# Kernel tuning notes

Measured on AMD Instinct MI355X. Metric: run time of the kernel, lower is better.

The kernel has to match this reference:

```python
import jax, jax.numpy as jnp
import numpy as np

B, Cin, H, W = 8, 256, 32, 32
KS, NH, K = 32, 8, 5          # key_size == value_size, num_heads, kernel_size
STRIDE, PAD = 1, 2
Cout = KS * 3 * NH            # 768
EPS = 1e-5


def setup_inputs() -> dict:
    key = jax.random.key(0)
    k0, k1, k2 = jax.random.split(key, 3)
    return {
        "x": jax.random.normal(k0, (B, Cin, H, W), jnp.float32),
        "conv_w": jax.random.normal(k1, (Cout, Cin), jnp.float32) / np.sqrt(Cin).astype(np.float32),
        "conv_b": jax.random.normal(k2, (Cout,), jnp.float32) * 0.02,
        "gn_w": jnp.ones((Cout,), jnp.float32),
        "gn_b": jnp.zeros((Cout,), jnp.float32),
    }


def reference(x, conv_w, conv_b, gn_w, gn_b):
    Bb = x.shape[0]
    OH = (H + 2 * PAD - K) // STRIDE + 1
    OW = (W + 2 * PAD - K) // STRIDE + 1

    # 1x1 conv: (B, Cout, H, W)
    attn = jnp.einsum('bchw,oc->bohw', x, conv_w) + conv_b[None, :, None, None]

    # unfold / Tile2d -> (B, KH, KW, Cout, OH, OW)
    ap = jnp.pad(attn, ((0, 0), (0, 0), (PAD, PAD), (PAD, PAD)))
    rows = []
    for kh in range(K):
        cols = [ap[:, :, kh:kh + OH * STRIDE:STRIDE, kw:kw + OW * STRIDE:STRIDE]
                for kw in range(K)]
        rows.append(jnp.stack(cols, axis=1))          # (B, KW, C, OH, OW)
    tiles = jnp.stack(rows, axis=1)                   # (B, KH, KW, C, OH, OW)

    # GroupNorm over (group_channels, OH, OW) per (b, kh, kw) sample.
    # groups = 3*NH, group size = KS (each head's key/query/value chunk).
    G = 3 * NH
    t = tiles.reshape(Bb, K, K, G, KS, OH, OW)
    mean = t.mean(axis=(4, 5, 6), keepdims=True)
    var = t.var(axis=(4, 5, 6), keepdims=True)        # biased, like torch GroupNorm
    t = (t - mean) * jax.lax.rsqrt(var + EPS)
    t = t.reshape(Bb, K, K, Cout, OH, OW)
    t = t * gn_w[None, None, None, :, None, None] + gn_b[None, None, None, :, None, None]

    # (B, OH, OW, NH, 3*KS, KH*KW)
    t = t.transpose(0, 4, 5, 3, 1, 2).reshape(Bb, OH, OW, NH, 3 * KS, K * K)
    keyt = t[..., :KS, :]            # (B, OH, OW, NH, KS, KK)
    qt = t[..., KS:2 * KS, :]
    vt = t[..., 2 * KS:, :]          # (B, OH, OW, NH, VS, KK)

    q = qt.mean(axis=-1)             # mean query over the window: (B, OH, OW, NH, KS)
    sal = jnp.einsum('bijnk,bijnkp->bijnp', q, keyt) / np.float32(np.sqrt(KS))
    mask = jax.nn.softmax(sal, axis=-1)               # (B, OH, OW, NH, KK)
    out = jnp.einsum('bijnvp,bijnp->bijnv', vt, mask)  # (B, OH, OW, NH, VS)

    out = out.transpose(0, 3, 4, 1, 2).reshape(Bb, NH * KS, OH, OW)
    return out
```

## Files before the change

kernel.cpp:

```cpp
#include <hip/hip_runtime.h>
#include <hip/hip_bf16.h>

#define B_    8
#define CIN   256
#define COUT  768
#define G_    24
#define PW    40
#define PLANE 1440
#define EPS_  1e-5f

typedef float f32x4 __attribute__((ext_vector_type(4)));
typedef short s16x8 __attribute__((ext_vector_type(8)));
typedef unsigned short ushort_t;
typedef unsigned short u16x4 __attribute__((ext_vector_type(4)));
typedef unsigned long long ull_t;

static __device__ __forceinline__ ushort_t f2bf(float f) {
    union { float f; unsigned u; } a; a.f = f;
    const unsigned u = a.u;
    const unsigned r = u + 0x7FFFu + ((u >> 16) & 1u);
    return (ushort_t)(r >> 16);
}
static __device__ __forceinline__ float bf2f(ushort_t h) {
    union { unsigned u; float f; } a; a.u = ((unsigned)h) << 16; return a.f;
}

__launch_bounds__(256)
__global__ void prep(const float* __restrict__ x, const float* __restrict__ w,
                     ushort_t* __restrict__ Xt, ushort_t* __restrict__ Wt) {
    const int z = blockIdx.x;
    const int t = threadIdx.x;
    if (z < 2048) {
        __shared__ ushort_t tile[32][33];
        const int b  = z >> 8, rem = z & 255;
        const int k0 = (rem >> 5) * 32, n0 = (rem & 31) * 32;
        const int kk = t >> 5, nn = t & 31;
        #pragma unroll
        for (int it = 0; it < 4; ++it) {
            const int kr = kk + it * 8;
            tile[kr][nn] = f2bf(x[((size_t)(b * 256 + k0 + kr)) * 1024 + n0 + nn]);
        }
        __syncthreads();
        const int kk2 = t & 31, nb = t >> 5;
        #pragma unroll
        for (int it = 0; it < 4; ++it) {
            const int nr = nb + it * 8;
            Xt[((size_t)(b * 1024 + n0 + nr)) * 256 + k0 + kk2] = tile[kk2][nr];
        }
    } else {
        const int idx = (z - 2048) * 256 + t;
        Wt[idx] = f2bf(w[idx]);
    }
}

__launch_bounds__(256)
__global__ void conv_gemm(const ushort_t* __restrict__ Wt, const ushort_t* __restrict__ Xt,
                          const float* __restrict__ bias, ushort_t* __restrict__ attn,
                          float* __restrict__ rowAgg) {
    const int t = threadIdx.x;
    const int wv = t >> 6, lane = t & 63;
    const int q = lane >> 4, l15 = lane & 15;
    const int m0 = blockIdx.y * 64;
    const int mw = wv * 16;
    const int n_t = blockIdx.x * 64;
    const int b = n_t >> 10, nl0 = n_t & 1023;
    const int y0 = nl0 >> 5;

    __shared__ ushort_t Ct[64][2][44];
    __shared__ float red[128][11];

    const ushort_t* aP = Wt + (size_t)(m0 + mw + l15) * 256 + q * 8;
    const ushort_t* bP = Xt + (size_t)(b * 1024 + nl0 + l15) * 256 + q * 8;

    f32x4 acc[4] = {{0,0,0,0},{0,0,0,0},{0,0,0,0},{0,0,0,0}};
    #pragma unroll
    for (int k0 = 0; k0 < 256; k0 += 32) {
        const s16x8 a  = *(const s16x8*)(aP + k0);
        const s16x8 b0 = *(const s16x8*)(bP + k0);
        const s16x8 b1 = *(const s16x8*)(bP + 16 * 256 + k0);
        const s16x8 b2 = *(const s16x8*)(bP + 32 * 256 + k0);
        const s16x8 b3 = *(const s16x8*)(bP + 48 * 256 + k0);
        acc[0] = __builtin_amdgcn_mfma_f32_16x16x32_bf16(a, b0, acc[0], 0, 0, 0);
        acc[1] = __builtin_amdgcn_mfma_f32_16x16x32_bf16(a, b1, acc[1], 0, 0, 0);
        acc[2] = __builtin_amdgcn_mfma_f32_16x16x32_bf16(a, b2, acc[2], 0, 0, 0);
        acc[3] = __builtin_amdgcn_mfma_f32_16x16x32_bf16(a, b3, acc[3], 0, 0, 0);
    }

    float bb[4];
    #pragma unroll
    for (int r = 0; r < 4; ++r) bb[r] = bias[m0 + mw + q * 4 + r];
    #pragma unroll
    for (int j = 0; j < 4; ++j) {
        const int yy = j >> 1, xx = (j & 1) * 16 + l15;
        #pragma unroll
        for (int r = 0; r < 4; ++r)
            Ct[mw + q * 4 + r][yy][2 + xx] = f2bf(acc[j][r] + bb[r]);
    }
    #pragma unroll
    for (int it = 0; it < 2; ++it) {
        const int id = it * 256 + t;
        const int m = id >> 3, yy = (id >> 2) & 1, pos = id & 3;
        const int us = (pos == 0) ? 0 : (32 + 2 * pos);
        *(unsigned*)&Ct[m][yy][us] = 0u;
    }
    __syncthreads();

    ushort_t* pb = attn + ((size_t)(b * COUT + m0)) * PLANE;
    #pragma unroll
    for (int it = 0; it < 5; ++it) {
        const int id = it * 256 + t;
        const int m = id / 20, rem = id % 20, yy = rem / 10, s = rem % 10;
        const ull_t v = *(const ull_t*)&Ct[m][yy][s * 4];
        *(ull_t*)(pb + (size_t)m * PLANE + (y0 + yy + 2) * PW + s * 4) = v;
    }
    if (y0 == 0 || y0 == 30) {
        const int rowA = (y0 == 0) ? 0 : 34;
        #pragma unroll
        for (int it = 0; it < 5; ++it) {
            const int id = it * 256 + t;
            const int m = id / 20, rem = id % 20, yy = rem / 10, s = rem % 10;
            *(ull_t*)(pb + (size_t)m * PLANE + (rowA + yy) * PW + s * 4) = 0ull;
        }
    }

    if (t < 128) {
        const int gi = t >> 6, yy = (t >> 5) & 1, c = t & 31;
        const int m = gi * 32 + c;
        float lin = 0.f, sq = 0.f, e0 = 0.f, e1 = 0.f, e30 = 0.f, e31 = 0.f;
        #pragma unroll
        for (int u = 0; u < 9; ++u) {
            const ull_t vv = *(const ull_t*)&Ct[m][yy][u * 4];
            const unsigned lo = (unsigned)vv, hi = (unsigned)(vv >> 32);
            union { unsigned u; float f; } f0, f1, f2, f3;
            f0.u = lo << 16; f1.u = lo & 0xffff0000u;
            f2.u = hi << 16; f3.u = hi & 0xffff0000u;
            lin += (f0.f + f1.f) + (f2.f + f3.f);
            sq  += (f0.f * f0.f + f1.f * f1.f) + (f2.f * f2.f + f3.f * f3.f);
            if (u == 0) { e0 = f2.f; e1 = f3.f; }
            if (u == 8) { e30 = f0.f; e31 = f1.f; }
        }
        red[t][0] = lin; red[t][1] = sq;
        red[t][2] = e0;  red[t][3] = e0 * e0;
        red[t][4] = e1;  red[t][5] = e1 * e1;
        red[t][6] = e30; red[t][7] = e30 * e30;
        red[t][8] = e31; red[t][9] = e31 * e31;
    }
    __syncthreads();
    if (t < 40) {
        const int s = t % 10, gy = t / 10;
        const int gi = gy >> 1, yy = gy & 1;
        float sum = 0.f;
        #pragma unroll
        for (int c = 0; c < 32; ++c) sum += red[gi * 64 + yy * 32 + c][s];
        const int g = blockIdx.y * 2 + gi;
        rowAgg[(((size_t)b * G_ + g) * 32 + (y0 + yy)) * 10 + s] = sum;
    }
}

__launch_bounds__(64)
__global__ void gnfin(const float* __restrict__ rowAgg,
                      float* __restrict__ meanArr, float* __restrict__ rstdArr) {
    const int bg = blockIdx.x;
    const int t = threadIdx.x;
    __shared__ float rp[32][5], rp2[32][5];
    if (t < 32) {
        const float* a = rowAgg + ((size_t)bg * 32 + t) * 10;
        const float S = a[0], Sq = a[1];
        const float e0 = a[2], q0 = a[3], e1 = a[4], q1 = a[5];
        const float e30 = a[6], q30 = a[7], e31 = a[8], q31 = a[9];
        rp[t][0] = S - e30 - e31; rp[t][1] = S - e31; rp[t][2] = S;
        rp[t][3] = S - e0;        rp[t][4] = S - e0 - e1;
        rp2[t][0] = Sq - q30 - q31; rp2[t][1] = Sq - q31; rp2[t][2] = Sq;
        rp2[t][3] = Sq - q0;        rp2[t][4] = Sq - q0 - q1;
    }
    __syncthreads();
    if (t < 25) {
        const int kw = t % 5, kh = t / 5;
        float cs = 0.f, cs2 = 0.f;
        #pragma unroll
        for (int yy = 0; yy < 32; ++yy) { cs += rp[yy][kw]; cs2 += rp2[yy][kw]; }
        if (kh == 0)      { cs -= rp[30][kw] + rp[31][kw]; cs2 -= rp2[30][kw] + rp2[31][kw]; }
        else if (kh == 1) { cs -= rp[31][kw];              cs2 -= rp2[31][kw]; }
        else if (kh == 3) { cs -= rp[0][kw];               cs2 -= rp2[0][kw]; }
        else if (kh == 4) { cs -= rp[0][kw] + rp[1][kw];   cs2 -= rp2[0][kw] + rp2[1][kw]; }
        const float inv_n = 1.f / 32768.f;
        const float mean = cs * inv_n;
        const float var  = cs2 * inv_n - mean * mean;
        meanArr[bg * 25 + t] = mean;
        rstdArr[bg * 25 + t] = rsqrtf(var + EPS_);
    }
}

__launch_bounds__(256, 1)
__global__ void local_attn(const ushort_t* __restrict__ attn,
                           const float* __restrict__ meanArr, const float* __restrict__ rstdArr,
                           const float* __restrict__ gn_w, const float* __restrict__ gn_b,
                           float* __restrict__ out) {
    const int blk = blockIdx.x;
    const int b = blk >> 5;
    const int n = (blk >> 2) & 7;
    const int slab = blk & 3;
    const int i0 = slab * 8;
    const int t = threadIdx.x;
    const int r = t >> 5, j = t & 31;

    __shared__ float Ks[2][480];
    __shared__ float Qs[2][480];
    __shared__ float Vs[2][960];
    __shared__ float s_rq[25], s_mq[25], s_rk[25], s_ck[25], s_rv[25], s_cv[25];
    __shared__ float s_gw[96], s_gb[96];

    if (t < 25) {
        const int gk = (b * G_ + n * 3) * 25 + t;
        const float mK = meanArr[gk],      rK = rstdArr[gk];
        const float mQ = meanArr[gk + 25], rQ = rstdArr[gk + 25];
        const float mV = meanArr[gk + 50], rV = rstdArr[gk + 50];
        s_rk[t] = rK; s_ck[t] = mK * rK;
        s_rq[t] = rQ; s_mq[t] = mQ * rQ;
        s_rv[t] = rV; s_cv[t] = mV * rV;
    }
    if (t < 96) { s_gw[t] = gn_w[n * 96 + t]; s_gb[t] = gn_b[n * 96 + t]; }
    __syncthreads();

    float rq[25]; float cQ = 0.f;
    #pragma unroll
    for (int p = 0; p < 25; ++p) { rq[p] = s_rq[p]; cQ += s_mq[p]; }

    const ushort_t* aB = attn + (size_t)(b * COUT + n * 96) * PLANE + i0 * PW;
    const bool stg = (t < 240);
    const int sp = (t < 120) ? 0 : 1;
    const int eo = ((t < 120) ? t : (t - 120)) * 4;

    u16x4 vr = {0, 0, 0, 0};
    if (stg) vr = *(const u16x4*)(aB + (size_t)(sp * 32) * PLANE + eo);

    float sal[25];
    #pragma unroll
    for (int p = 0; p < 25; ++p) sal[p] = 0.f;
    float sumQ2 = 0.f, sumQB = 0.f;

    const int base = r * PW + j;

    for (int ch = 0; ch < 32; ++ch) {
        const int buf = ch & 1;
        if (stg) {
            f32x4 w4 = { bf2f(vr[0]), bf2f(vr[1]), bf2f(vr[2]), bf2f(vr[3]) };
            if (sp == 0) *(f32x4*)&Ks[buf][eo] = w4;
            else         *(f32x4*)&Qs[buf][eo] = w4;
        }
        __syncthreads();
        if (stg) {
            if (ch < 31) vr = *(const u16x4*)(aB + (size_t)(ch + 1 + sp * 32) * PLANE + eo);
            else         vr = *(const u16x4*)(aB + (size_t)(64 + sp) * PLANE + eo);
        }
        const float* qb = &Qs[buf][base];
        const float* kb = &Ks[buf][base];
        float qa0 = 0.f, qa1 = 0.f, qa2 = 0.f, qa3 = 0.f, qa4 = 0.f;
        #pragma unroll
        for (int kw = 0; kw < 5; ++kw) {
            qa0 += rq[0 * 5 + kw] * qb[0 * PW + kw];
            qa1 += rq[1 * 5 + kw] * qb[1 * PW + kw];
            qa2 += rq[2 * 5 + kw] * qb[2 * PW + kw];
            qa3 += rq[3 * 5 + kw] * qb[3 * PW + kw];
            qa4 += rq[4 * 5 + kw] * qb[4 * PW + kw];
        }
        const float qa = (qa0 + qa1) + (qa2 + qa3) + qa4;
        const float qk  = s_gw[32 + ch] * ((qa - cQ) * 0.04f) + s_gb[32 + ch];
        const float qk2 = qk * s_gw[ch];
        sumQ2 += qk2; sumQB += qk * s_gb[ch];
        #pragma unroll
        for (int kh = 0; kh < 5; ++kh)
            #pragma unroll
            for (int kw = 0; kw < 5; ++kw)
                sal[kh * 5 + kw] += qk2 * kb[kh * PW + kw];
    }

    #pragma unroll
    for (int p = 0; p < 25; ++p) sal[p] = s_rk[p] * sal[p] - s_ck[p] * sumQ2 + sumQB;

    const float scale = 0.17677669529663687f;
    float mmax = -3.4e38f;
    #pragma unroll
    for (int p = 0; p < 25; ++p) { sal[p] *= scale; mmax = fmaxf(mmax, sal[p]); }
    float ssum = 0.f;
    #pragma unroll
    for (int p = 0; p < 25; ++p) { sal[p] = __expf(sal[p] - mmax); ssum += sal[p]; }
    const float rs = 1.f / ssum;
    float w2[25]; float cV2 = 0.f;
    #pragma unroll
    for (int p = 0; p < 25; ++p) {
        const float m = sal[p] * rs;
        w2[p] = m * s_rv[p];
        cV2 += m * s_cv[p];
    }

    for (int vi = 0; vi < 16; ++vi) {
        const int buf = vi & 1;
        if (stg) {
            f32x4 w4 = { bf2f(vr[0]), bf2f(vr[1]), bf2f(vr[2]), bf2f(vr[3]) };
            *(f32x4*)&Vs[buf][sp * 480 + eo] = w4;
        }
        __syncthreads();
        if (stg && vi < 15)
            vr = *(const u16x4*)(aB + (size_t)(64 + 2 * (vi + 1) + sp) * PLANE + eo);
        #pragma unroll
        for (int h = 0; h < 2; ++h) {
            const float* vb = &Vs[buf][h * 480 + base];
            float a0 = 0.f, a1 = 0.f, a2 = 0.f, a3 = 0.f, a4 = 0.f;
            #pragma unroll
            for (int kw = 0; kw < 5; ++kw) {
                a0 += w2[0 * 5 + kw] * vb[0 * PW + kw];
                a1 += w2[1 * 5 + kw] * vb[1 * PW + kw];
                a2 += w2[2 * 5 + kw] * vb[2 * PW + kw];
                a3 += w2[3 * 5 + kw] * vb[3 * PW + kw];
                a4 += w2[4 * 5 + kw] * vb[4 * PW + kw];
            }
            const float acc = (a0 + a1) + (a2 + a3) + a4;
            const int v = vi * 2 + h;
            out[((size_t)(b * 256 + n * 32 + v) * 32 + (i0 + r)) * 32 + j] =
                s_gw[64 + v] * acc + (s_gb[64 + v] - s_gw[64 + v] * cV2);
        }
    }
}

extern "C" void kernel_launch(void* const* d_in, const int* in_sizes, int n_in,
                              void* d_out, int out_size, void* d_ws, size_t ws_size,
                              hipStream_t stream) {
    const float* x      = (const float*)d_in[0];
    const float* conv_w = (const float*)d_in[1];
    const float* conv_b = (const float*)d_in[2];
    const float* gn_w   = (const float*)d_in[3];
    const float* gn_b   = (const float*)d_in[4];
    float* out = (float*)d_out;

    ushort_t* attn    = (ushort_t*)d_ws;
    ushort_t* Xt      = attn + 8847360;
    ushort_t* Wt      = Xt + 2097152;
    float*    rowAgg  = (float*)(Wt + 196608);
    float*    meanArr = rowAgg + 61440;
    float*    rstdArr = meanArr + 4800;

    prep<<<2816, 256, 0, stream>>>(x, conv_w, Xt, Wt);
    conv_gemm<<<dim3(128, 12), 256, 0, stream>>>(Wt, Xt, conv_b, attn, rowAgg);
    gnfin<<<192, 64, 0, stream>>>(rowAgg, meanArr, rstdArr);
    local_attn<<<256, 256, 0, stream>>>(attn, meanArr, rstdArr, gn_w, gn_b, out);
}
```

Measured before the change: 133.4 us.

## Split local_attn into 1024 single-wave blocks of two rows each

The local attention kernel moves from 256 blocks of 256 threads, each covering 8 output rows, to 1024 blocks of 64 threads, each covering 2 rows. The goal is to spread work across more CUs and shrink per-block sync cost. Staging changes from a double buffer to a single buffer with a two-deep register prefetch and two barriers per channel, and the V buffer now reuses the K buffer. Each block now loads 6 halo rows for 2 output rows instead of 12 for 8, so redundant global reads rise.

```diff
diff --git a/kernel.cpp b/kernel.cpp
--- a/kernel.cpp
+++ b/kernel.cpp
@@ -191,22 +191,22 @@
     }
 }
 
-__launch_bounds__(256, 1)
+__launch_bounds__(64)
 __global__ void local_attn(const ushort_t* __restrict__ attn,
                            const float* __restrict__ meanArr, const float* __restrict__ rstdArr,
                            const float* __restrict__ gn_w, const float* __restrict__ gn_b,
                            float* __restrict__ out) {
     const int blk = blockIdx.x;
-    const int b = blk >> 5;
-    const int n = (blk >> 2) & 7;
-    const int slab = blk & 3;
-    const int i0 = slab * 8;
+    const int b = blk >> 7;
+    const int n = (blk >> 4) & 7;
+    const int slab = blk & 15;
+    const int i0 = slab * 2;
     const int t = threadIdx.x;
     const int r = t >> 5, j = t & 31;
-
-    __shared__ float Ks[2][480];
-    __shared__ float Qs[2][480];
-    __shared__ float Vs[2][960];
+    const int row = i0 + r;
+
+    __shared__ float KB[240];
+    __shared__ float QB[240];
     __shared__ float s_rq[25], s_mq[25], s_rk[25], s_ck[25], s_rv[25], s_cv[25];
     __shared__ float s_gw[96], s_gb[96];
 
@@ -219,42 +219,56 @@
         s_rq[t] = rQ; s_mq[t] = mQ * rQ;
         s_rv[t] = rV; s_cv[t] = mV * rV;
     }
-    if (t < 96) { s_gw[t] = gn_w[n * 96 + t]; s_gb[t] = gn_b[n * 96 + t]; }
+    s_gw[t] = gn_w[n * 96 + t];
+    s_gb[t] = gn_b[n * 96 + t];
+    if (t < 32) {
+        s_gw[64 + t] = gn_w[n * 96 + 64 + t];
+        s_gb[64 + t] = gn_b[n * 96 + 64 + t];
+    }
     __syncthreads();
 
     float rq[25]; float cQ = 0.f;
     #pragma unroll
     for (int p = 0; p < 25; ++p) { rq[p] = s_rq[p]; cQ += s_mq[p]; }
 
-    const ushort_t* aB = attn + (size_t)(b * COUT + n * 96) * PLANE + i0 * PW;
-    const bool stg = (t < 240);
-    const int sp = (t < 120) ? 0 : 1;
-    const int eo = ((t < 120) ? t : (t - 120)) * 4;
-
-    u16x4 vr = {0, 0, 0, 0};
-    if (stg) vr = *(const u16x4*)(aB + (size_t)(sp * 32) * PLANE + eo);
+    const ushort_t* regB = attn + (size_t)(b * COUT + n * 96) * PLANE + i0 * PW;
+    const bool stg = (t < 60);
+    const int eo = t * 4;
+    const int base = r * PW + j;
+
+    const ushort_t* baseK = regB;
+    const ushort_t* baseQ = regB + (size_t)32 * PLANE;
+    const ushort_t* baseV = regB + (size_t)64 * PLANE;
+
+    u16x4 pK0 = {0,0,0,0}, pK1 = {0,0,0,0}, pQ0 = {0,0,0,0}, pQ1 = {0,0,0,0};
+    if (stg) {
+        pK0 = *(const u16x4*)(baseK + eo);
+        pQ0 = *(const u16x4*)(baseQ + eo);
+        pK1 = *(const u16x4*)(baseK + PLANE + eo);
+        pQ1 = *(const u16x4*)(baseQ + PLANE + eo);
+    }
 
     float sal[25];
     #pragma unroll
     for (int p = 0; p < 25; ++p) sal[p] = 0.f;
     float sumQ2 = 0.f, sumQB = 0.f;
 
-    const int base = r * PW + j;
-
+    #pragma unroll 2
     for (int ch = 0; ch < 32; ++ch) {
-        const int buf = ch & 1;
         if (stg) {
-            f32x4 w4 = { bf2f(vr[0]), bf2f(vr[1]), bf2f(vr[2]), bf2f(vr[3]) };
-            if (sp == 0) *(f32x4*)&Ks[buf][eo] = w4;
-            else         *(f32x4*)&Qs[buf][eo] = w4;
-        }
-        __syncthreads();
-        if (stg) {
-            if (ch < 31) vr = *(const u16x4*)(aB + (size_t)(ch + 1 + sp * 32) * PLANE + eo);
-            else         vr = *(const u16x4*)(aB + (size_t)(64 + sp) * PLANE + eo);
-        }
-        const float* qb = &Qs[buf][base];
-        const float* kb = &Ks[buf][base];
+            f32x4 k4 = { bf2f(pK0[0]), bf2f(pK0[1]), bf2f(pK0[2]), bf2f(pK0[3]) };
+            f32x4 q4 = { bf2f(pQ0[0]), bf2f(pQ0[1]), bf2f(pQ0[2]), bf2f(pQ0[3]) };
+            *(f32x4*)&KB[eo] = k4;
+            *(f32x4*)&QB[eo] = q4;
+            pK0 = pK1; pQ0 = pQ1;
+            if (ch < 30) {
+                pK1 = *(const u16x4*)(baseK + (size_t)(ch + 2) * PLANE + eo);
+                pQ1 = *(const u16x4*)(baseQ + (size_t)(ch + 2) * PLANE + eo);
+            }
+        }
+        __syncthreads();
+        const float* qb = &QB[base];
+        const float* kb = &KB[base];
         float qa0 = 0.f, qa1 = 0.f, qa2 = 0.f, qa3 = 0.f, qa4 = 0.f;
         #pragma unroll
         for (int kw = 0; kw < 5; ++kw) {
@@ -273,6 +287,13 @@
             #pragma unroll
             for (int kw = 0; kw < 5; ++kw)
                 sal[kh * 5 + kw] += qk2 * kb[kh * PW + kw];
+        __syncthreads();
+    }
+
+    u16x4 pV0 = {0,0,0,0}, pV1 = {0,0,0,0};
+    if (stg) {
+        pV0 = *(const u16x4*)(baseV + eo);
+        pV1 = *(const u16x4*)(baseV + PLANE + eo);
     }
 
     #pragma unroll
@@ -286,40 +307,37 @@
     #pragma unroll
     for (int p = 0; p < 25; ++p) { sal[p] = __expf(sal[p] - mmax); ssum += sal[p]; }
     const float rs = 1.f / ssum;
-    float w2[25]; float cV2 = 0.f;
+    float cV2 = 0.f;
     #pragma unroll
     for (int p = 0; p < 25; ++p) {
         const float m = sal[p] * rs;
-        w2[p] = m * s_rv[p];
+        sal[p] = m * s_rv[p];
         cV2 += m * s_cv[p];
     }
 
-    for (int vi = 0; vi < 16; ++vi) {
-        const int buf = vi & 1;
+    #pragma unroll 2
+    for (int v = 0; v < 32; ++v) {
         if (stg) {
-            f32x4 w4 = { bf2f(vr[0]), bf2f(vr[1]), bf2f(vr[2]), bf2f(vr[3]) };
-            *(f32x4*)&Vs[buf][sp * 480 + eo] = w4;
-        }
-        __syncthreads();
-        if (stg && vi < 15)
-            vr = *(const u16x4*)(aB + (size_t)(64 + 2 * (vi + 1) + sp) * PLANE + eo);
-        #pragma unroll
-        for (int h = 0; h < 2; ++h) {
-            const float* vb = &Vs[buf][h * 480 + base];
-            float a0 = 0.f, a1 = 0.f, a2 = 0.f, a3 = 0.f, a4 = 0.f;
-            #pragma unroll
-            for (int kw = 0; kw < 5; ++kw) {
-                a0 += w2[0 * 5 + kw] * vb[0 * PW + kw];
-                a1 += w2[1 * 5 + kw] * vb[1 * PW + kw];
-                a2 += w2[2 * 5 + kw] * vb[2 * PW + kw];
-                a3 += w2[3 * 5 + kw] * vb[3 * PW + kw];
-                a4 += w2[4 * 5 + kw] * vb[4 * PW + kw];
-            }
-            const float acc = (a0 + a1) + (a2 + a3) + a4;
-            const int v = vi * 2 + h;
-            out[((size_t)(b * 256 + n * 32 + v) * 32 + (i0 + r)) * 32 + j] =
-                s_gw[64 + v] * acc + (s_gb[64 + v] - s_gw[64 + v] * cV2);
-        }
+            f32x4 v4 = { bf2f(pV0[0]), bf2f(pV0[1]), bf2f(pV0[2]), bf2f(pV0[3]) };
+            *(f32x4*)&KB[eo] = v4;
+            pV0 = pV1;
+            if (v < 30) pV1 = *(const u16x4*)(baseV + (size_t)(v + 2) * PLANE + eo);
+        }
+        __syncthreads();
+        const float* vb = &KB[base];
+        float a0 = 0.f, a1 = 0.f, a2 = 0.f, a3 = 0.f, a4 = 0.f;
+        #pragma unroll
+        for (int kw = 0; kw < 5; ++kw) {
+            a0 += sal[0 * 5 + kw] * vb[0 * PW + kw];
+            a1 += sal[1 * 5 + kw] * vb[1 * PW + kw];
+            a2 += sal[2 * 5 + kw] * vb[2 * PW + kw];
+            a3 += sal[3 * 5 + kw] * vb[3 * PW + kw];
+            a4 += sal[4 * 5 + kw] * vb[4 * PW + kw];
+        }
+        const float acc = (a0 + a1) + (a2 + a3) + a4;
+        out[((size_t)(b * 256 + n * 32 + v) * 32 + row) * 32 + j] =
+            s_gw[64 + v] * acc + (s_gb[64 + v] - s_gw[64 + v] * cV2);
+        __syncthreads();
     }
 }
 
@@ -343,5 +361,5 @@
     prep<<<2816, 256, 0, stream>>>(x, conv_w, Xt, Wt);
     conv_gemm<<<dim3(128, 12), 256, 0, stream>>>(Wt, Xt, conv_b, attn, rowAgg);
     gnfin<<<192, 64, 0, stream>>>(rowAgg, meanArr, rstdArr);
-    local_attn<<<256, 256, 0, stream>>>(attn, meanArr, rstdArr, gn_w, gn_b, out);
-}
+    local_attn<<<1024, 64, 0, stream>>>(attn, meanArr, rstdArr, gn_w, gn_b, out);
+}
```

After: 143.7 us. +7.8%, slower.
